# Performance work log

Hardware: AMD Instinct MI355X
Metric: run time of the kernel (lower is better)

## Reference

```python
import jax, jax.numpy as jnp
import numpy as np

N, M, F0, FB, F, H, NC, NCONV = 60000, 12, 92, 41, 64, 128, 2000, 3
EPS = 1e-5


def setup_inputs() -> dict:
    key = jax.random.key(0)
    ks = jax.random.split(key, 12)
    s = 0.05
    return {
        "atom_fea": jax.random.normal(ks[0], (N, F0), jnp.float32),
        "nbr_fea": jax.random.normal(ks[1], (N, M, FB), jnp.float32),
        "nbr_fea_idx": jax.random.randint(ks[2], (N, M), 0, N),
        "crystal_atom_idx": jnp.sort(jax.random.randint(ks[3], (N,), 0, NC)),
        "W_emb": jax.random.normal(ks[4], (F0, F), jnp.float32) * s,
        "b_emb": jnp.zeros((F,), jnp.float32),
        "W_full": jax.random.normal(ks[5], (NCONV, 2 * F + FB, 2 * F), jnp.float32) * s,
        "b_full": jnp.zeros((NCONV, 2 * F), jnp.float32),
        "g1": jnp.ones((NCONV, 2 * F), jnp.float32),
        "be1": jnp.zeros((NCONV, 2 * F), jnp.float32),
        "g2": jnp.ones((NCONV, F), jnp.float32),
        "be2": jnp.zeros((NCONV, F), jnp.float32),
        "W_fc": jax.random.normal(ks[6], (F, H), jnp.float32) * s,
        "b_fc": jnp.zeros((H,), jnp.float32),
        "W_out": jax.random.normal(ks[7], (H, 1), jnp.float32) * s,
        "b_out": jnp.zeros((1,), jnp.float32),
    }


def _bn(x, g, b):
    # training-mode batch norm over leading (row) dim
    m = x.mean(axis=0)
    v = x.var(axis=0)
    return (x - m) * jax.lax.rsqrt(v + EPS) * g + b


def _conv_layer(x, nbr_fea, nbr_fea_idx, Wf, bf, g1, be1, g2, be2):
    n, m = nbr_fea_idx.shape
    f = x.shape[1]
    atom_nbr = x[nbr_fea_idx]  # (N, M, F) gather
    total = jnp.concatenate(
        [jnp.broadcast_to(x[:, None, :], (n, m, f)), atom_nbr, nbr_fea], axis=2
    )  # (N, M, 2F+FB)
    gated = total @ Wf + bf  # (N, M, 2F)
    gated = _bn(gated.reshape(-1, 2 * f), g1, be1).reshape(n, m, 2 * f)
    nbr_filter, nbr_core = jnp.split(gated, 2, axis=2)
    summed = jnp.sum(jax.nn.sigmoid(nbr_filter) * jax.nn.softplus(nbr_core), axis=1)
    summed = _bn(summed, g2, be2)
    return jax.nn.softplus(x + summed)


def reference(atom_fea, nbr_fea, nbr_fea_idx, crystal_atom_idx, W_emb, b_emb,
              W_full, b_full, g1, be1, g2, be2, W_fc, b_fc, W_out, b_out):
    x = atom_fea @ W_emb + b_emb  # (N, F)
    for i in range(NCONV):
        x = _conv_layer(x, nbr_fea, nbr_fea_idx, W_full[i], b_full[i],
                        g1[i], be1[i], g2[i], be2[i])
    # mean-pool atoms per crystal (segment mean)
    sums = jax.ops.segment_sum(x, crystal_atom_idx, num_segments=NC)
    cnt = jax.ops.segment_sum(jnp.ones((x.shape[0],), x.dtype), crystal_atom_idx,
                              num_segments=NC)
    crys = sums / jnp.maximum(cnt, 1.0)[:, None]  # (NC, F)
    crys = jax.nn.softplus(crys) @ W_fc + b_fc
    crys = jax.nn.softplus(crys)
    return crys @ W_out + b_out  # (NC, 1)
```

## Files before the change

kernel.cpp:

```cpp
#include <hip/hip_runtime.h>
#include <hip/hip_bf16.h>


#define NATOM 60000
#define MNBR  12
#define F0D   92
#define FBD   41
#define FD    64
#define F2D   128
#define NCRY  2000
#define HD    128
#define NSUP  15000
#define GS    132

#define OFF_X      0ull
#define OFF_XH     3840000ull
#define OFF_SUMMED 5760000ull
#define OFF_STATS  9600000ull
#define OFF_CRYS   9600384ull
#define OFF_CNT    9728384ull
#define OFF_WCONV  9730384ull
#define OFF_WBF    9811220ull
#define OFF_FLAG   9848084ull
#define WS_NEED_BYTES (9848085ull * 4ull)
#define OFF_BPAD   9848088ull
#define WS_FULL_BYTES ((OFF_BPAD + 17280000ull) * 4ull)

#define W_EMB_O  0
#define B_EMB_O  5888
#define W_FULL_O 5952
#define B_FULL_O 70848
#define G1_O     71232
#define BE1_O    71616
#define G2_O     72000
#define BE2_O    72192
#define W_FC_O   72384
#define B_FC_O   80576
#define W_OUT_O  80704
#define B_OUT_O  80832
#define WC_TOTAL 80833

typedef unsigned short u16;
typedef __attribute__((ext_vector_type(8))) short bf16x8;
typedef __attribute__((ext_vector_type(4))) float f32x4;

__device__ __forceinline__ float bf2f(u16 u){
  union { unsigned int i; float f; } v; v.i = ((unsigned int)u) << 16; return v.f;
}
__device__ __forceinline__ u16 f2bf(float f){
  union { float f; unsigned int i; } v; v.f = f;
  unsigned int x = v.i;
  return (u16)((x + 0x7FFFu + ((x >> 16) & 1u)) >> 16);
}
__device__ __forceinline__ float softplusf_(float x){
  return fmaxf(x, 0.f) + log1pf(expf(-fabsf(x)));
}
__device__ __forceinline__ float softplus_fast(float x){
  return fmaxf(x, 0.f) + __logf(1.f + __expf(-fabsf(x)));
}
__device__ __forceinline__ float sigmoid_fast(float x){
  return __builtin_amdgcn_rcpf(1.f + __expf(-x));
}

__global__ __launch_bounds__(64) void detect_kernel(
    const u16* __restrict__ data, int* __restrict__ flag){
  int tid = threadIdx.x;
  float v = bf2f(data[tid * 2]);
  float av = fabsf(v);
  bool sane = (av > 1e-6f) && (av < 100.f);
  unsigned long long m = __ballot(sane);
  if (tid == 0) *flag = (__popcll(m) >= 32) ? 1 : 0;
}

struct CvtArgs {
  const void* src[12];
  int start[13];
};

__global__ __launch_bounds__(256) void cvt_all_kernel(
    CvtArgs a, float* __restrict__ dst, const int* __restrict__ flag){
  int i = blockIdx.x * 256 + threadIdx.x;
  if (i >= WC_TOTAL) return;
  int r = 0;
  while (i >= a.start[r + 1]) r++;
  int rel = i - a.start[r];
  if (*flag) dst[i] = bf2f(((const u16*)a.src[r])[rel]);
  else       dst[i] = ((const float*)a.src[r])[rel];
}

__global__ __launch_bounds__(256) void build_bfrag(
    const float* __restrict__ wfull, u16* __restrict__ wbf){
  int t = blockIdx.x * 256 + threadIdx.x;
  if (t >= 3 * 6 * 8 * 64) return;
  int lane = t & 63, nt = (t >> 6) & 7, c = (t >> 9) % 6, layer = t / 3072;
  int q = lane >> 4, nloc = lane & 15;
  u16 vals[8];
  #pragma unroll
  for (int i = 0; i < 8; i++){
    int k = c * 32 + q * 8 + i;
    float v = (k < 169) ? wfull[layer * 169 * F2D + k * F2D + nt * 16 + nloc] : 0.f;
    vals[i] = f2bf(v);
  }
  *(uint4*)&wbf[(size_t)t * 8] = *(uint4*)vals;
}

__global__ __launch_bounds__(256) void bond_prep(
    const void* __restrict__ nbr_fea, u16* __restrict__ bond_pad,
    const int* __restrict__ flag){
  __shared__ __align__(16) char sm[7872];
  u16*   lb_u = (u16*)sm;
  float* lb_f = (float*)sm;
  int s = blockIdx.x, tid = threadIdx.x;
  const int isbf = *flag;
  if (isbf){
    const uint4* src = (const uint4*)((const u16*)nbr_fea + (size_t)s * 1968);
    if (tid < 246) ((uint4*)sm)[tid] = src[tid];
  } else {
    const uint4* src = (const uint4*)((const float*)nbr_fea + (size_t)s * 1968);
    for (int t = tid; t < 492; t += 256) ((uint4*)sm)[t] = src[t];
  }
  __syncthreads();
  uint4* outv = (uint4*)(bond_pad + (size_t)s * 2304);
  for (int slot = tid; slot < 288; slot += 256){
    int et = slot / 96, jj = slot - et * 96;
    int l  = (jj < 64) ? jj : (jj - 64);
    int row = et * 16 + (l & 15);
    int kb  = ((jj < 64) ? 0 : 32) + (l >> 4) * 8;
    u16 v[8];
    #pragma unroll
    for (int i = 0; i < 8; i++){
      int k = kb + i;
      v[i] = (k < FBD) ? (isbf ? lb_u[row * FBD + k] : f2bf(lb_f[row * FBD + k])) : (u16)0;
    }
    outv[slot] = *(uint4*)v;
  }
}

__global__ __launch_bounds__(256) void embed_kernel(
    const void* __restrict__ atom_fea, const float* __restrict__ W_emb,
    const float* __restrict__ b_emb, float* __restrict__ x,
    u16* __restrict__ xh, const int* __restrict__ flag){
  int tid = threadIdx.x;
  int n = blockIdx.x * 4 + (tid >> 6);
  int f = tid & 63;
  float acc = b_emb[f];
  if (*flag){
    const u16* arow = (const u16*)atom_fea + n * F0D;
    for (int k = 0; k < F0D; k++)
      acc = fmaf(bf2f(arow[k]), W_emb[k * FD + f], acc);
  } else {
    const float* arow = (const float*)atom_fea + n * F0D;
    for (int k = 0; k < F0D; k++)
      acc = fmaf(arow[k], W_emb[k * FD + f], acc);
  }
  x[n * FD + f] = acc;
  xh[n * FD + f] = f2bf(acc);
}

template<int ACT>
__global__ __launch_bounds__(256, 3) void conv_share(
    const u16* __restrict__ xh, const u16* __restrict__ bond_pad,
    const int* __restrict__ nbr_idx, const u16* __restrict__ wbf_l,
    const float* __restrict__ bfull, const float* __restrict__ sum1,
    const float* __restrict__ sq1, const float* __restrict__ g1,
    const float* __restrict__ be1, float* __restrict__ summed,
    float* __restrict__ o_sum, float* __restrict__ o_sq){
  extern __shared__ char smem[];
  char* stg  = smem;
  float* gbuf = (float*)(smem + 11264);
  float* redS = ACT ? (gbuf + 48 * GS) : (float*)(smem + 11264);
  float* redQ = redS + (ACT ? 64 : 128);

  const int tid = threadIdx.x;
  const int w = tid >> 6, lane = tid & 63;
  const int q = lane >> 4, nloc = lane & 15;

  bf16x8 Bf[6][2];
  const bf16x8* Bv = (const bf16x8*)wbf_l;
  #pragma unroll
  for (int c = 0; c < 6; c++)
    #pragma unroll
    for (int t2 = 0; t2 < 2; t2++)
      Bf[c][t2] = Bv[(c * 8 + w * 2 + t2) * 64 + lane];
  float bias0 = bfull[w * 32 + nloc];
  float bias1 = bfull[w * 32 + 16 + nloc];

  float A0 = 0.f, B0 = 0.f, A1 = 0.f, B1 = 0.f;
  if (ACT){
    const float invR = 1.f / (float)(NATOM * MNBR);
    float m0 = sum1[lane] * invR;
    float v0 = fmaxf(sq1[lane] * invR - m0 * m0, 0.f);
    A0 = g1[lane] * rsqrtf(v0 + 1e-5f);  B0 = be1[lane] - m0 * A0;
    float m1 = sum1[64 + lane] * invR;
    float v1 = fmaxf(sq1[64 + lane] * invR - m1 * m1, 0.f);
    A1 = g1[64 + lane] * rsqrtf(v1 + 1e-5f);  B1 = be1[64 + lane] - m1 * A1;
  }
  float sAcc0 = 0.f, sAcc1 = 0.f, qAcc0 = 0.f, qAcc1 = 0.f;
  if (tid < (ACT ? 64 : 128)){ redS[tid] = 0.f; redQ[tid] = 0.f; }

  const char* xh8   = (const char*)xh;
  const char* bpad8 = (const char*)bond_pad;
  const int jx1 = tid - 64;
  const int rA  = (tid >= 64) ? ((jx1 >> 7) * 16 + (jx1 & 15)) : 0;
  const int cg1 = (tid >= 64) ? ((((jx1 >> 6) & 1) * 4 + ((jx1 >> 4) & 3)) * 16) : 0;
  const int jx2 = tid + 192;
  const int rB  = (tid < 192) ? ((jx2 >> 7) * 16 + (jx2 & 15)) : 0;
  const int cg2 = (tid < 192) ? ((((jx2 >> 6) & 1) * 4 + ((jx2 >> 4) & 3)) * 16) : 0;

  const int na_off0 = nloc / 12;
  const int na_off1 = (16 + nloc) / 12;
  const int na_off2 = (32 + nloc) / 12;

  const bf16x8 zero8 = {0,0,0,0,0,0,0,0};

  for (int s = blockIdx.x; s < NSUP; s += gridDim.x){
    {
      int nbA = nbr_idx[s * 48 + rA];
      int nbB = nbr_idx[s * 48 + rB];
      uint4 rb = *(const uint4*)(bpad8 + (size_t)s * 4608 + (size_t)tid * 16);
      const char* p1;
      if (tid < 32)      p1 = bpad8 + (size_t)s * 4608 + (size_t)(tid + 256) * 16;
      else if (tid < 64) p1 = xh8 + (size_t)s * 512 + (size_t)(tid - 32) * 16;
      else               p1 = xh8 + (size_t)nbA * 128 + cg1;
      uint4 r1 = *(const uint4*)p1;
      *(uint4*)(stg + tid * 16) = rb;
      *(uint4*)(stg + 4096 + tid * 16) = r1;
      if (tid < 192){
        uint4 r2 = *(const uint4*)(xh8 + (size_t)nbB * 128 + cg2);
        *(uint4*)(stg + 8192 + tid * 16) = r2;
      }
    }
    __syncthreads();

    #pragma unroll
    for (int et = 0; et < 3; et++){
      int naloc = (et == 0) ? na_off0 : (et == 1) ? na_off1 : na_off2;
      const char* xs = stg + 4608 + naloc * 128;
      bf16x8 a0 = *(const bf16x8*)(xs + q * 16);
      bf16x8 a1 = *(const bf16x8*)(xs + 64 + q * 16);
      bf16x8 a2 = *(const bf16x8*)(stg + 5120 + (et * 128 + lane) * 16);
      bf16x8 a3 = *(const bf16x8*)(stg + 5120 + (et * 128 + 64 + lane) * 16);
      bf16x8 a4 = *(const bf16x8*)(stg + (et * 96 + lane) * 16);
      bf16x8 a5 = (lane < 32) ? *(const bf16x8*)(stg + (et * 96 + 64 + lane) * 16)
                              : zero8;
      #pragma unroll
      for (int t2 = 0; t2 < 2; t2++){
        float bs = t2 ? bias1 : bias0;
        f32x4 acc = {bs, bs, bs, bs};
        acc = __builtin_amdgcn_mfma_f32_16x16x32_bf16(a0, Bf[0][t2], acc, 0, 0, 0);
        acc = __builtin_amdgcn_mfma_f32_16x16x32_bf16(a1, Bf[1][t2], acc, 0, 0, 0);
        acc = __builtin_amdgcn_mfma_f32_16x16x32_bf16(a2, Bf[2][t2], acc, 0, 0, 0);
        acc = __builtin_amdgcn_mfma_f32_16x16x32_bf16(a3, Bf[3][t2], acc, 0, 0, 0);
        acc = __builtin_amdgcn_mfma_f32_16x16x32_bf16(a4, Bf[4][t2], acc, 0, 0, 0);
        acc = __builtin_amdgcn_mfma_f32_16x16x32_bf16(a5, Bf[5][t2], acc, 0, 0, 0);
        if (ACT){
          int col = w * 32 + t2 * 16 + nloc;
          int r0 = et * 16 + q * 4;
          gbuf[(r0 + 0) * GS + col] = acc[0];
          gbuf[(r0 + 1) * GS + col] = acc[1];
          gbuf[(r0 + 2) * GS + col] = acc[2];
          gbuf[(r0 + 3) * GS + col] = acc[3];
        } else {
          float ss = acc[0] + acc[1] + acc[2] + acc[3];
          float qq = acc[0]*acc[0] + acc[1]*acc[1] + acc[2]*acc[2] + acc[3]*acc[3];
          if (t2){ sAcc1 += ss; qAcc1 += qq; } else { sAcc0 += ss; qAcc0 += qq; }
        }
      }
    }
    if (ACT){
      __syncthreads();
      float p = 0.f;
      #pragma unroll
      for (int m = 0; m < 12; m++){
        int el = w * 12 + m;
        float u = fmaf(gbuf[el * GS + lane],      A0, B0);
        float v = fmaf(gbuf[el * GS + 64 + lane], A1, B1);
        p = fmaf(sigmoid_fast(u), softplus_fast(v), p);
      }
      summed[((size_t)s * 4 + w) * 64 + lane] = p;
      sAcc0 += p;  qAcc0 = fmaf(p, p, qAcc0);
    }
    __syncthreads();
  }

  if (ACT){
    atomicAdd(&redS[lane], sAcc0);
    atomicAdd(&redQ[lane], qAcc0);
    __syncthreads();
    if (tid < 64){ atomicAdd(&o_sum[tid], redS[tid]); atomicAdd(&o_sq[tid], redQ[tid]); }
  } else {
    int c0 = w * 32 + nloc;
    atomicAdd(&redS[c0], sAcc0);       atomicAdd(&redQ[c0], qAcc0);
    atomicAdd(&redS[c0 + 16], sAcc1);  atomicAdd(&redQ[c0 + 16], qAcc1);
    __syncthreads();
    if (tid < 128){ atomicAdd(&o_sum[tid], redS[tid]); atomicAdd(&o_sq[tid], redQ[tid]); }
  }
}

template<int ACT>
__global__ __launch_bounds__(256, 3) void conv_mfma(
    const u16* __restrict__ xh, const void* __restrict__ nbr_fea,
    const int* __restrict__ nbr_idx, const u16* __restrict__ wbf_l,
    const float* __restrict__ bfull, const float* __restrict__ sum1,
    const float* __restrict__ sq1, const float* __restrict__ g1,
    const float* __restrict__ be1, float* __restrict__ summed,
    float* __restrict__ o_sum, float* __restrict__ o_sq,
    const int* __restrict__ flag){
  extern __shared__ char smem[];
  u16*   fragA = (u16*)smem;
  float* gbuf  = (float*)(smem + 6144);
  float* redS  = ACT ? (gbuf + 48 * GS) : (float*)(smem + 6144);
  float* redQ  = redS + (ACT ? 64 : 128);

  const int tid = threadIdx.x;
  const int w = tid >> 6, lane = tid & 63;
  const int q = lane >> 4, nloc = lane & 15, q8 = q * 8;
  const int isbf = *flag;

  bf16x8 Bf[6][2];
  const bf16x8* Bv = (const bf16x8*)wbf_l;
  #pragma unroll
  for (int c = 0; c < 6; c++)
    #pragma unroll
    for (int t2 = 0; t2 < 2; t2++)
      Bf[c][t2] = Bv[(c * 8 + w * 2 + t2) * 64 + lane];
  float bias0 = bfull[w * 32 + nloc];
  float bias1 = bfull[w * 32 + 16 + nloc];

  float A0 = 0.f, B0 = 0.f, A1 = 0.f, B1 = 0.f;
  if (ACT){
    const float invR = 1.f / (float)(NATOM * MNBR);
    float m0 = sum1[lane] * invR;
    float v0 = fmaxf(sq1[lane] * invR - m0 * m0, 0.f);
    A0 = g1[lane] * rsqrtf(v0 + 1e-5f);  B0 = be1[lane] - m0 * A0;
    float m1 = sum1[64 + lane] * invR;
    float v1 = fmaxf(sq1[64 + lane] * invR - m1 * m1, 0.f);
    A1 = g1[64 + lane] * rsqrtf(v1 + 1e-5f);  B1 = be1[64 + lane] - m1 * A1;
  }
  float sAcc0 = 0.f, sAcc1 = 0.f, qAcc0 = 0.f, qAcc1 = 0.f;
  if (tid < (ACT ? 64 : 128)){ redS[tid] = 0.f; redQ[tid] = 0.f; }

  const bf16x8* xv = (const bf16x8*)xh;
  for (int s = blockIdx.x; s < NSUP; s += gridDim.x){
    int e0 = s * 48 + nloc;
    int nb0 = nbr_idx[e0], nb1 = nbr_idx[e0 + 16], nb2 = nbr_idx[e0 + 32];
    bf16x8 Af[3][6];
    if (w < 3){
      size_t eg = (size_t)(s * 48 + w * 16 + nloc);
      u16 v4[8], v5[8];
      if (isbf){
        const u16* br = (const u16*)nbr_fea + eg * 41;
        #pragma unroll
        for (int i = 0; i < 8; i++) v4[i] = br[q8 + i];
        #pragma unroll
        for (int i = 0; i < 8; i++){
          int k5 = 32 + q8 + i;
          v5[i] = (k5 < 41) ? br[k5] : (u16)0;
        }
      } else {
        const float* br = (const float*)nbr_fea + eg * 41;
        #pragma unroll
        for (int i = 0; i < 8; i++) v4[i] = f2bf(br[q8 + i]);
        #pragma unroll
        for (int i = 0; i < 8; i++){
          int k5 = 32 + q8 + i;
          v5[i] = (k5 < 41) ? f2bf(br[k5]) : (u16)0;
        }
      }
      *(uint4*)&fragA[(w * 2 + 0) * 512 + lane * 8] = *(uint4*)v4;
      *(uint4*)&fragA[(w * 2 + 1) * 512 + lane * 8] = *(uint4*)v5;
    }
    __syncthreads();
    #pragma unroll
    for (int et = 0; et < 3; et++){
      int nb = (et == 0) ? nb0 : (et == 1) ? nb1 : nb2;
      int na = s * 4 + (et * 16 + nloc) / 12;
      Af[et][0] = xv[na * 8 + q];
      Af[et][1] = xv[na * 8 + 4 + q];
      Af[et][2] = xv[nb * 8 + q];
      Af[et][3] = xv[nb * 8 + 4 + q];
      Af[et][4] = *(bf16x8*)&fragA[(et * 2 + 0) * 512 + lane * 8];
      Af[et][5] = *(bf16x8*)&fragA[(et * 2 + 1) * 512 + lane * 8];
    }
    #pragma unroll
    for (int et = 0; et < 3; et++){
      #pragma unroll
      for (int t2 = 0; t2 < 2; t2++){
        float bs = t2 ? bias1 : bias0;
        f32x4 acc = {bs, bs, bs, bs};
        acc = __builtin_amdgcn_mfma_f32_16x16x32_bf16(Af[et][0], Bf[0][t2], acc, 0, 0, 0);
        acc = __builtin_amdgcn_mfma_f32_16x16x32_bf16(Af[et][1], Bf[1][t2], acc, 0, 0, 0);
        acc = __builtin_amdgcn_mfma_f32_16x16x32_bf16(Af[et][2], Bf[2][t2], acc, 0, 0, 0);
        acc = __builtin_amdgcn_mfma_f32_16x16x32_bf16(Af[et][3], Bf[3][t2], acc, 0, 0, 0);
        acc = __builtin_amdgcn_mfma_f32_16x16x32_bf16(Af[et][4], Bf[4][t2], acc, 0, 0, 0);
        acc = __builtin_amdgcn_mfma_f32_16x16x32_bf16(Af[et][5], Bf[5][t2], acc, 0, 0, 0);
        if (ACT){
          int col = w * 32 + t2 * 16 + nloc;
          int r0 = et * 16 + q * 4;
          gbuf[(r0 + 0) * GS + col] = acc[0];
          gbuf[(r0 + 1) * GS + col] = acc[1];
          gbuf[(r0 + 2) * GS + col] = acc[2];
          gbuf[(r0 + 3) * GS + col] = acc[3];
        } else {
          float ss = acc[0] + acc[1] + acc[2] + acc[3];
          float qq = acc[0]*acc[0] + acc[1]*acc[1] + acc[2]*acc[2] + acc[3]*acc[3];
          if (t2){ sAcc1 += ss; qAcc1 += qq; } else { sAcc0 += ss; qAcc0 += qq; }
        }
      }
    }
    if (ACT){
      __syncthreads();
      float p = 0.f;
      #pragma unroll
      for (int m = 0; m < 12; m++){
        int el = w * 12 + m;
        float u = fmaf(gbuf[el * GS + lane],      A0, B0);
        float v = fmaf(gbuf[el * GS + 64 + lane], A1, B1);
        p = fmaf(sigmoid_fast(u), softplus_fast(v), p);
      }
      summed[(s * 4 + w) * 64 + lane] = p;
      sAcc0 += p;  qAcc0 = fmaf(p, p, qAcc0);
    }
    __syncthreads();
  }
  if (ACT){
    atomicAdd(&redS[lane], sAcc0);
    atomicAdd(&redQ[lane], qAcc0);
    __syncthreads();
    if (tid < 64){ atomicAdd(&o_sum[tid], redS[tid]); atomicAdd(&o_sq[tid], redQ[tid]); }
  } else {
    int c0 = w * 32 + nloc;
    atomicAdd(&redS[c0], sAcc0);       atomicAdd(&redQ[c0], qAcc0);
    atomicAdd(&redS[c0 + 16], sAcc1);  atomicAdd(&redQ[c0 + 16], qAcc1);
    __syncthreads();
    if (tid < 128){ atomicAdd(&o_sum[tid], redS[tid]); atomicAdd(&o_sq[tid], redQ[tid]); }
  }
}

__global__ __launch_bounds__(256) void update_x_kernel(
    float* __restrict__ x, u16* __restrict__ xh,
    const float* __restrict__ summed,
    const float* __restrict__ sum2, const float* __restrict__ sq2,
    const float* __restrict__ g2, const float* __restrict__ be2){
  int idx = blockIdx.x * 256 + threadIdx.x;
  int f = idx & 63;
  const float invN = 1.f / (float)NATOM;
  float mean = sum2[f] * invN;
  float var  = fmaxf(sq2[f] * invN - mean * mean, 0.f);
  float a = g2[f] * rsqrtf(var + 1e-5f);
  float b = be2[f] - mean * a;
  float v = x[idx] + fmaf(summed[idx], a, b);
  float r = softplusf_(v);
  x[idx] = r;
  xh[idx] = f2bf(r);
}

__global__ __launch_bounds__(256) void pool_kernel(
    const float* __restrict__ x, const int* __restrict__ cidx,
    float* __restrict__ crys, float* __restrict__ cnt){
  int idx = blockIdx.x * 256 + threadIdx.x;
  int n = idx >> 6, f = idx & 63;
  int c = cidx[n];
  atomicAdd(&crys[c * FD + f], x[idx]);
  if (f == 0) atomicAdd(&cnt[c], 1.f);
}

__global__ __launch_bounds__(128) void head_kernel(
    const float* __restrict__ crys, const float* __restrict__ cnt,
    const float* __restrict__ W_fc, const float* __restrict__ b_fc,
    const float* __restrict__ W_out, const float* __restrict__ b_out,
    void* __restrict__ out, const int* __restrict__ flag){
  __shared__ float p_s[FD];
  __shared__ float red_s[HD];
  int c = blockIdx.x, tid = threadIdx.x;
  if (tid < FD){
    float ct = fmaxf(cnt[c], 1.f);
    p_s[tid] = softplusf_(crys[c * FD + tid] / ct);
  }
  __syncthreads();
  float acc = b_fc[tid];
  for (int k = 0; k < FD; k++)
    acc = fmaf(p_s[k], W_fc[k * HD + tid], acc);
  float h = softplusf_(acc);
  red_s[tid] = h * W_out[tid];
  __syncthreads();
  for (int s = HD / 2; s > 0; s >>= 1){
    if (tid < s) red_s[tid] += red_s[tid + s];
    __syncthreads();
  }
  if (tid == 0){
    float r = red_s[0] + b_out[0];
    if (*flag) ((u16*)out)[c] = f2bf(r);
    else       ((float*)out)[c] = r;
  }
}

extern "C" void kernel_launch(void* const* d_in, const int* in_sizes, int n_in,
                              void* d_out, int out_size, void* d_ws, size_t ws_size,
                              hipStream_t stream){
  if (ws_size < WS_NEED_BYTES) return;
  const bool full = (ws_size >= WS_FULL_BYTES);
  const void* atom_fea = d_in[0];
  const void* nbr_fea  = d_in[1];
  const int* nbr_idx   = (const int*)d_in[2];
  const int* cidx      = (const int*)d_in[3];

  float* ws     = (float*)d_ws;
  float* x      = ws + OFF_X;
  u16*   xh     = (u16*)(ws + OFF_XH);
  float* summed = ws + OFF_SUMMED;
  float* sum1   = ws + OFF_STATS;
  float* sq1    = sum1 + 128;
  float* sum2   = sq1 + 128;
  float* sq2    = sum2 + 64;
  float* crys   = ws + OFF_CRYS;
  float* cnt    = ws + OFF_CNT;
  float* wc     = ws + OFF_WCONV;
  u16*   wbf    = (u16*)(ws + OFF_WBF);
  int*   flag   = (int*)(ws + OFF_FLAG);
  u16*   bpad   = (u16*)(ws + OFF_BPAD);

  detect_kernel<<<1, 64, 0, stream>>>((const u16*)nbr_fea, flag);
  CvtArgs ca;
  const int srcidx[12] = {4,5,6,7,8,9,10,11,12,13,14,15};
  const int starts[13] = {W_EMB_O, B_EMB_O, W_FULL_O, B_FULL_O, G1_O, BE1_O,
                          G2_O, BE2_O, W_FC_O, B_FC_O, W_OUT_O, B_OUT_O, WC_TOTAL};
  for (int i = 0; i < 12; i++){ ca.src[i] = d_in[srcidx[i]]; ca.start[i] = starts[i]; }
  ca.start[12] = WC_TOTAL;
  cvt_all_kernel<<<(WC_TOTAL + 255) / 256, 256, 0, stream>>>(ca, wc, flag);
  build_bfrag<<<(9216 + 255) / 256, 256, 0, stream>>>(wc + W_FULL_O, wbf);
  if (full) bond_prep<<<NSUP, 256, 0, stream>>>(nbr_fea, bpad, flag);

  embed_kernel<<<NATOM / 4, 256, 0, stream>>>(atom_fea, wc + W_EMB_O, wc + B_EMB_O,
                                              x, xh, flag);
  const int LDS_STATS_S = 11264 + 2 * 128 * 4;
  const int LDS_ACT_S   = 11264 + (48 * GS + 128) * 4;
  const int LDS_STATS_F = 6144 + 2 * 128 * 4;
  const int LDS_ACT_F   = 6144 + (48 * GS + 128) * 4;
  for (int i = 0; i < 3; i++){
    const u16* wbf_l = wbf + (size_t)i * 3072 * 8;
    hipMemsetAsync(sum1, 0, 384 * sizeof(float), stream);
    if (full){
      conv_share<0><<<3000, 256, LDS_STATS_S, stream>>>(xh, bpad, nbr_idx,
          wbf_l, wc + B_FULL_O + i * F2D, sum1, sq1, wc + G1_O + i * F2D,
          wc + BE1_O + i * F2D, summed, sum1, sq1);
      conv_share<1><<<3000, 256, LDS_ACT_S, stream>>>(xh, bpad, nbr_idx,
          wbf_l, wc + B_FULL_O + i * F2D, sum1, sq1, wc + G1_O + i * F2D,
          wc + BE1_O + i * F2D, summed, sum2, sq2);
    } else {
      conv_mfma<0><<<3000, 256, LDS_STATS_F, stream>>>(xh, nbr_fea, nbr_idx,
          wbf_l, wc + B_FULL_O + i * F2D, sum1, sq1, wc + G1_O + i * F2D,
          wc + BE1_O + i * F2D, summed, sum1, sq1, flag);
      conv_mfma<1><<<3000, 256, LDS_ACT_F, stream>>>(xh, nbr_fea, nbr_idx,
          wbf_l, wc + B_FULL_O + i * F2D, sum1, sq1, wc + G1_O + i * F2D,
          wc + BE1_O + i * F2D, summed, sum2, sq2, flag);
    }
    update_x_kernel<<<(NATOM * FD) / 256, 256, 0, stream>>>(x, xh, summed, sum2, sq2,
        wc + G2_O + i * FD, wc + BE2_O + i * FD);
  }
  hipMemsetAsync(crys, 0, (NCRY * FD + NCRY) * sizeof(float), stream);
  pool_kernel<<<(NATOM * FD) / 256, 256, 0, stream>>>(x, cidx, crys, cnt);
  head_kernel<<<NCRY, 128, 0, stream>>>(crys, cnt, wc + W_FC_O, wc + B_FC_O,
      wc + W_OUT_O, wc + B_OUT_O, d_out, flag);
}
```

Measured before the change: 998.6 us.

## Pair filter/core columns per wave and fuse gating into MFMA epilogue

Reorders the neighbour-row layout in the bond buffer and the gather indices so each MFMA output row group holds one atom's neighbours. Each wave now computes the matching filter and core column tiles, so the sigmoid*softplus gating and the neighbour sum run directly on accumulator registers. This removes the 48x132 LDS staging buffer, one barrier and the LDS round trip per super-tile, and shrinks LDS use. The cost is that each thread now holds a more intricate index mapping that must exactly match the bond_prep layout.

```diff
diff --git a/kernel.cpp b/kernel.cpp
--- a/kernel.cpp
+++ b/kernel.cpp
@@ -124,7 +124,8 @@
   for (int slot = tid; slot < 288; slot += 256){
     int et = slot / 96, jj = slot - et * 96;
     int l  = (jj < 64) ? jj : (jj - 64);
-    int row = et * 16 + (l & 15);
+    int tr = l & 15;
+    int row = (tr >> 2) * 12 + et * 4 + (tr & 3);
     int kb  = ((jj < 64) ? 0 : 32) + (l >> 4) * 8;
     u16 v[8];
     #pragma unroll
@@ -158,7 +159,7 @@
 }
 
 template<int ACT>
-__global__ __launch_bounds__(256, 3) void conv_share(
+__global__ __launch_bounds__(256, 3) void conv_fused(
     const u16* __restrict__ xh, const u16* __restrict__ bond_pad,
     const int* __restrict__ nbr_idx, const u16* __restrict__ wbf_l,
     const float* __restrict__ bfull, const float* __restrict__ sum1,
@@ -167,49 +168,47 @@
     float* __restrict__ o_sum, float* __restrict__ o_sq){
   extern __shared__ char smem[];
   char* stg  = smem;
-  float* gbuf = (float*)(smem + 11264);
-  float* redS = ACT ? (gbuf + 48 * GS) : (float*)(smem + 11264);
+  float* redS = (float*)(smem + 11264);
   float* redQ = redS + (ACT ? 64 : 128);
 
   const int tid = threadIdx.x;
   const int w = tid >> 6, lane = tid & 63;
   const int q = lane >> 4, nloc = lane & 15;
+  const int cf = w * 16 + nloc;
 
   bf16x8 Bf[6][2];
   const bf16x8* Bv = (const bf16x8*)wbf_l;
   #pragma unroll
-  for (int c = 0; c < 6; c++)
-    #pragma unroll
-    for (int t2 = 0; t2 < 2; t2++)
-      Bf[c][t2] = Bv[(c * 8 + w * 2 + t2) * 64 + lane];
-  float bias0 = bfull[w * 32 + nloc];
-  float bias1 = bfull[w * 32 + 16 + nloc];
+  for (int c = 0; c < 6; c++){
+    Bf[c][0] = Bv[(c * 8 + w) * 64 + lane];
+    Bf[c][1] = Bv[(c * 8 + 4 + w) * 64 + lane];
+  }
+  const float bias0 = bfull[cf];
+  const float bias1 = bfull[64 + cf];
 
   float A0 = 0.f, B0 = 0.f, A1 = 0.f, B1 = 0.f;
   if (ACT){
     const float invR = 1.f / (float)(NATOM * MNBR);
-    float m0 = sum1[lane] * invR;
-    float v0 = fmaxf(sq1[lane] * invR - m0 * m0, 0.f);
-    A0 = g1[lane] * rsqrtf(v0 + 1e-5f);  B0 = be1[lane] - m0 * A0;
-    float m1 = sum1[64 + lane] * invR;
-    float v1 = fmaxf(sq1[64 + lane] * invR - m1 * m1, 0.f);
-    A1 = g1[64 + lane] * rsqrtf(v1 + 1e-5f);  B1 = be1[64 + lane] - m1 * A1;
-  }
-  float sAcc0 = 0.f, sAcc1 = 0.f, qAcc0 = 0.f, qAcc1 = 0.f;
+    float m0 = sum1[cf] * invR;
+    float v0 = fmaxf(sq1[cf] * invR - m0 * m0, 0.f);
+    A0 = g1[cf] * rsqrtf(v0 + 1e-5f);       B0 = be1[cf] - m0 * A0;
+    float m1 = sum1[64 + cf] * invR;
+    float v1 = fmaxf(sq1[64 + cf] * invR - m1 * m1, 0.f);
+    A1 = g1[64 + cf] * rsqrtf(v1 + 1e-5f);  B1 = be1[64 + cf] - m1 * A1;
+  }
+  float sAcc0 = 0.f, qAcc0 = 0.f, sAcc1 = 0.f, qAcc1 = 0.f;
   if (tid < (ACT ? 64 : 128)){ redS[tid] = 0.f; redQ[tid] = 0.f; }
 
   const char* xh8   = (const char*)xh;
   const char* bpad8 = (const char*)bond_pad;
   const int jx1 = tid - 64;
-  const int rA  = (tid >= 64) ? ((jx1 >> 7) * 16 + (jx1 & 15)) : 0;
+  const int rA  = (tid >= 64)
+      ? (((jx1 & 15) >> 2) * 12 + (jx1 >> 7) * 4 + (jx1 & 3)) : 0;
   const int cg1 = (tid >= 64) ? ((((jx1 >> 6) & 1) * 4 + ((jx1 >> 4) & 3)) * 16) : 0;
   const int jx2 = tid + 192;
-  const int rB  = (tid < 192) ? ((jx2 >> 7) * 16 + (jx2 & 15)) : 0;
+  const int rB  = (tid < 192)
+      ? (((jx2 & 15) >> 2) * 12 + (jx2 >> 7) * 4 + (jx2 & 3)) : 0;
   const int cg2 = (tid < 192) ? ((((jx2 >> 6) & 1) * 4 + ((jx2 >> 4) & 3)) * 16) : 0;
-
-  const int na_off0 = nloc / 12;
-  const int na_off1 = (16 + nloc) / 12;
-  const int na_off2 = (32 + nloc) / 12;
 
   const bf16x8 zero8 = {0,0,0,0,0,0,0,0};
 
@@ -232,10 +231,10 @@
     }
     __syncthreads();
 
+    float pa = 0.f;
     #pragma unroll
     for (int et = 0; et < 3; et++){
-      int naloc = (et == 0) ? na_off0 : (et == 1) ? na_off1 : na_off2;
-      const char* xs = stg + 4608 + naloc * 128;
+      const char* xs = stg + 4608 + (nloc >> 2) * 128;
       bf16x8 a0 = *(const bf16x8*)(xs + q * 16);
       bf16x8 a1 = *(const bf16x8*)(xs + 64 + q * 16);
       bf16x8 a2 = *(const bf16x8*)(stg + 5120 + (et * 128 + lane) * 16);
@@ -243,55 +242,49 @@
       bf16x8 a4 = *(const bf16x8*)(stg + (et * 96 + lane) * 16);
       bf16x8 a5 = (lane < 32) ? *(const bf16x8*)(stg + (et * 96 + 64 + lane) * 16)
                               : zero8;
-      #pragma unroll
-      for (int t2 = 0; t2 < 2; t2++){
-        float bs = t2 ? bias1 : bias0;
-        f32x4 acc = {bs, bs, bs, bs};
-        acc = __builtin_amdgcn_mfma_f32_16x16x32_bf16(a0, Bf[0][t2], acc, 0, 0, 0);
-        acc = __builtin_amdgcn_mfma_f32_16x16x32_bf16(a1, Bf[1][t2], acc, 0, 0, 0);
-        acc = __builtin_amdgcn_mfma_f32_16x16x32_bf16(a2, Bf[2][t2], acc, 0, 0, 0);
-        acc = __builtin_amdgcn_mfma_f32_16x16x32_bf16(a3, Bf[3][t2], acc, 0, 0, 0);
-        acc = __builtin_amdgcn_mfma_f32_16x16x32_bf16(a4, Bf[4][t2], acc, 0, 0, 0);
-        acc = __builtin_amdgcn_mfma_f32_16x16x32_bf16(a5, Bf[5][t2], acc, 0, 0, 0);
-        if (ACT){
-          int col = w * 32 + t2 * 16 + nloc;
-          int r0 = et * 16 + q * 4;
-          gbuf[(r0 + 0) * GS + col] = acc[0];
-          gbuf[(r0 + 1) * GS + col] = acc[1];
-          gbuf[(r0 + 2) * GS + col] = acc[2];
-          gbuf[(r0 + 3) * GS + col] = acc[3];
-        } else {
-          float ss = acc[0] + acc[1] + acc[2] + acc[3];
-          float qq = acc[0]*acc[0] + acc[1]*acc[1] + acc[2]*acc[2] + acc[3]*acc[3];
-          if (t2){ sAcc1 += ss; qAcc1 += qq; } else { sAcc0 += ss; qAcc0 += qq; }
+      f32x4 accF = {bias0, bias0, bias0, bias0};
+      accF = __builtin_amdgcn_mfma_f32_16x16x32_bf16(a0, Bf[0][0], accF, 0, 0, 0);
+      accF = __builtin_amdgcn_mfma_f32_16x16x32_bf16(a1, Bf[1][0], accF, 0, 0, 0);
+      accF = __builtin_amdgcn_mfma_f32_16x16x32_bf16(a2, Bf[2][0], accF, 0, 0, 0);
+      accF = __builtin_amdgcn_mfma_f32_16x16x32_bf16(a3, Bf[3][0], accF, 0, 0, 0);
+      accF = __builtin_amdgcn_mfma_f32_16x16x32_bf16(a4, Bf[4][0], accF, 0, 0, 0);
+      accF = __builtin_amdgcn_mfma_f32_16x16x32_bf16(a5, Bf[5][0], accF, 0, 0, 0);
+      f32x4 accC = {bias1, bias1, bias1, bias1};
+      accC = __builtin_amdgcn_mfma_f32_16x16x32_bf16(a0, Bf[0][1], accC, 0, 0, 0);
+      accC = __builtin_amdgcn_mfma_f32_16x16x32_bf16(a1, Bf[1][1], accC, 0, 0, 0);
+      accC = __builtin_amdgcn_mfma_f32_16x16x32_bf16(a2, Bf[2][1], accC, 0, 0, 0);
+      accC = __builtin_amdgcn_mfma_f32_16x16x32_bf16(a3, Bf[3][1], accC, 0, 0, 0);
+      accC = __builtin_amdgcn_mfma_f32_16x16x32_bf16(a4, Bf[4][1], accC, 0, 0, 0);
+      accC = __builtin_amdgcn_mfma_f32_16x16x32_bf16(a5, Bf[5][1], accC, 0, 0, 0);
+      if (ACT){
+        #pragma unroll
+        for (int i = 0; i < 4; i++){
+          float u = fmaf(accF[i], A0, B0);
+          float v = fmaf(accC[i], A1, B1);
+          pa = fmaf(sigmoid_fast(u), softplus_fast(v), pa);
         }
+      } else {
+        sAcc0 += accF[0] + accF[1] + accF[2] + accF[3];
+        qAcc0 += accF[0]*accF[0] + accF[1]*accF[1] + accF[2]*accF[2] + accF[3]*accF[3];
+        sAcc1 += accC[0] + accC[1] + accC[2] + accC[3];
+        qAcc1 += accC[0]*accC[0] + accC[1]*accC[1] + accC[2]*accC[2] + accC[3]*accC[3];
       }
     }
     if (ACT){
-      __syncthreads();
-      float p = 0.f;
-      #pragma unroll
-      for (int m = 0; m < 12; m++){
-        int el = w * 12 + m;
-        float u = fmaf(gbuf[el * GS + lane],      A0, B0);
-        float v = fmaf(gbuf[el * GS + 64 + lane], A1, B1);
-        p = fmaf(sigmoid_fast(u), softplus_fast(v), p);
-      }
-      summed[((size_t)s * 4 + w) * 64 + lane] = p;
-      sAcc0 += p;  qAcc0 = fmaf(p, p, qAcc0);
+      summed[((size_t)s * 4 + q) * 64 + cf] = pa;
+      sAcc0 += pa;  qAcc0 = fmaf(pa, pa, qAcc0);
     }
     __syncthreads();
   }
 
   if (ACT){
-    atomicAdd(&redS[lane], sAcc0);
-    atomicAdd(&redQ[lane], qAcc0);
+    atomicAdd(&redS[cf], sAcc0);
+    atomicAdd(&redQ[cf], qAcc0);
     __syncthreads();
     if (tid < 64){ atomicAdd(&o_sum[tid], redS[tid]); atomicAdd(&o_sq[tid], redQ[tid]); }
   } else {
-    int c0 = w * 32 + nloc;
-    atomicAdd(&redS[c0], sAcc0);       atomicAdd(&redQ[c0], qAcc0);
-    atomicAdd(&redS[c0 + 16], sAcc1);  atomicAdd(&redQ[c0 + 16], qAcc1);
+    atomicAdd(&redS[cf], sAcc0);       atomicAdd(&redQ[cf], qAcc0);
+    atomicAdd(&redS[64 + cf], sAcc1);  atomicAdd(&redQ[64 + cf], qAcc1);
     __syncthreads();
     if (tid < 128){ atomicAdd(&o_sum[tid], redS[tid]); atomicAdd(&o_sq[tid], redQ[tid]); }
   }
@@ -533,18 +526,18 @@
 
   embed_kernel<<<NATOM / 4, 256, 0, stream>>>(atom_fea, wc + W_EMB_O, wc + B_EMB_O,
                                               x, xh, flag);
-  const int LDS_STATS_S = 11264 + 2 * 128 * 4;
-  const int LDS_ACT_S   = 11264 + (48 * GS + 128) * 4;
+  const int LDS_STATS_N = 11264 + 2 * 128 * 4;
+  const int LDS_ACT_N   = 11264 + 2 * 64 * 4;
   const int LDS_STATS_F = 6144 + 2 * 128 * 4;
   const int LDS_ACT_F   = 6144 + (48 * GS + 128) * 4;
   for (int i = 0; i < 3; i++){
     const u16* wbf_l = wbf + (size_t)i * 3072 * 8;
     hipMemsetAsync(sum1, 0, 384 * sizeof(float), stream);
     if (full){
-      conv_share<0><<<3000, 256, LDS_STATS_S, stream>>>(xh, bpad, nbr_idx,
+      conv_fused<0><<<3000, 256, LDS_STATS_N, stream>>>(xh, bpad, nbr_idx,
           wbf_l, wc + B_FULL_O + i * F2D, sum1, sq1, wc + G1_O + i * F2D,
           wc + BE1_O + i * F2D, summed, sum1, sq1);
-      conv_share<1><<<3000, 256, LDS_ACT_S, stream>>>(xh, bpad, nbr_idx,
+      conv_fused<1><<<3000, 256, LDS_ACT_N, stream>>>(xh, bpad, nbr_idx,
           wbf_l, wc + B_FULL_O + i * F2D, sum1, sq1, wc + G1_O + i * F2D,
           wc + BE1_O + i * F2D, summed, sum2, sq2);
     } else {
```

After: 980.8 us. No clear change (-1.8%).
